# Performance work log

Hardware: AMD Instinct MI355X
Metric: run time of the kernel (lower is better)

Reference implementation:

```python
import jax, jax.numpy as jnp
import numpy as np


def conv3d(x, w, b, pad):
    # x: (B,C,D,H,W), w: (O,I,kd,kh,kw)
    y = jax.lax.conv_general_dilated(
        x, w, window_strides=(1, 1, 1), padding=[(pad, pad)] * 3,
        dimension_numbers=('NCDHW', 'OIDHW', 'NCDHW'))
    return y + b[None, :, None, None, None]


def setup_inputs() -> dict:
    key = jax.random.key(0)
    ks = jax.random.split(key, 8)
    B, C, D, H, W = 8, 128, 16, 32, 32
    C8 = C // 8
    return {
        'x': jax.random.normal(ks[0], (B, C, D, H, W), dtype=jnp.float32),
        'gamma': jax.random.normal(ks[1], (1,), dtype=jnp.float32),
        'w_k': jax.random.normal(ks[2], (C8, C, 1, 1, 1), dtype=jnp.float32) * 0.05,
        'b_k': jax.random.normal(ks[3], (C8,), dtype=jnp.float32) * 0.05,
        'w_q': jax.random.normal(ks[4], (C8, C, 1, 1, 1), dtype=jnp.float32) * 0.05,
        'b_q': jax.random.normal(ks[5], (C8,), dtype=jnp.float32) * 0.05,
        'w_v': jax.random.normal(ks[6], (C, C, 3, 3, 3), dtype=jnp.float32) * 0.02,
        'b_v': jax.random.normal(ks[7], (C,), dtype=jnp.float32) * 0.05,
    }


def reference(x, gamma, w_k, b_k, w_q, b_q, w_v, b_v):
    B, C, D, H, W = x.shape
    HW = H * W
    k = conv3d(x, w_k, b_k, 0)   # (B, C/8, D, H, W)
    q = conv3d(x, w_q, b_q, 0)   # (B, C/8, D, H, W)
    v = conv3d(x, w_v, b_v, 1)   # (B, C, D, H, W)

    # --- spatial (P) attention over HW positions, feature dim (C/8)*D ---
    kf = k.reshape(B, -1, HW)
    qf = q.reshape(B, -1, HW)
    # cor[b,s,t] = sum_f k[b,f,s] q[b,f,t]; softmax over t
    A_p = jax.nn.softmax(jnp.einsum('bfs,bft->bst', kf, qf), axis=-1)  # (B,HW,HW)
    vf = v.reshape(B, C * D, HW)
    # Patt[b,m,j] = sum_t v[b,m,t] A_p[b,j,t]  (v @ A_p^T)
    Patt = jnp.einsum('bmt,bjt->bmj', vf, A_p).reshape(B, C, D, H, W)

    # --- depth (D) attention over D slices, feature dim (C/8)*H*W ---
    kd = k.transpose(0, 2, 1, 3, 4).reshape(B, D, -1)
    qd = q.transpose(0, 2, 1, 3, 4).reshape(B, D, -1)
    A_d = jax.nn.softmax(jnp.einsum('bdf,bef->bde', kd, qd), axis=-1)  # (B,D,D)
    vd = v.transpose(0, 2, 1, 3, 4).reshape(B, D, -1)  # (B, D, C*H*W)
    # Datt[b,j,f] = sum_d A_d[b,j,d] vd[b,d,f]
    Datt = jnp.einsum('bjd,bdf->bjf', A_d, vd).reshape(B, D, C, H, W)
    Datt = Datt.transpose(0, 2, 1, 3, 4)  # (B,C,D,H,W)

    return gamma[0] * (Patt + Datt) + x
```

## Files before the change

### kernel.cpp

```cpp
#include <hip/hip_runtime.h>

#define HW   1024
#define DHW  16384

typedef __attribute__((ext_vector_type(8))) short short8;
typedef __attribute__((ext_vector_type(4))) float f32x4;

static __device__ __forceinline__ ushort f2bf(float f) {
  unsigned u = __float_as_uint(f);
  unsigned r = (u + 0x7fffu + ((u >> 16) & 1u)) >> 16;
  return (ushort)r;
}
static __device__ __forceinline__ float bf2f(ushort u) {
  return __uint_as_float(((unsigned)u) << 16);
}
static __device__ __forceinline__ void async_copy16(const ushort* g, ushort* l) {
  __builtin_amdgcn_global_load_lds(
      (const __attribute__((address_space(1))) unsigned int*)g,
      (__attribute__((address_space(3))) unsigned int*)l, 16, 0, 0);
}

__global__ __launch_bounds__(256) void kq_kernel(
    const float* __restrict__ x, const float* __restrict__ wk,
    const float* __restrict__ bk, const float* __restrict__ wq,
    const float* __restrict__ bq, float* __restrict__ k, float* __restrict__ q) {
  __shared__ float wks[16 * 128];
  __shared__ float wqs[16 * 128];
  int tid = threadIdx.x;
  for (int i = tid; i < 2048; i += 256) { wks[i] = wk[i]; wqs[i] = wq[i]; }
  __syncthreads();
  int b = blockIdx.y;
  int p = blockIdx.x * 256 + tid;
  float ak[16], aq[16];
#pragma unroll
  for (int o = 0; o < 16; ++o) { ak[o] = 0.f; aq[o] = 0.f; }
  const float* xb = x + (size_t)b * 128 * DHW + p;
  for (int c = 0; c < 128; ++c) {
    float xv = xb[(size_t)c * DHW];
#pragma unroll
    for (int o = 0; o < 16; ++o) {
      ak[o] += wks[o * 128 + c] * xv;
      aq[o] += wqs[o * 128 + c] * xv;
    }
  }
#pragma unroll
  for (int o = 0; o < 16; ++o) {
    k[((size_t)b * 16 + o) * DHW + p] = ak[o] + bk[o];
    q[((size_t)b * 16 + o) * DHW + p] = aq[o] + bq[o];
  }
}

__global__ __launch_bounds__(256) void wprep_kernel(
    const float* __restrict__ wv, ushort* __restrict__ wt,
    ushort* __restrict__ zbuf) {
  if (blockIdx.x == 0 && threadIdx.x < 512) zbuf[threadIdx.x] = 0;
  int i = blockIdx.x * 256 + threadIdx.x;
  if (i >= 27 * 128 * 128) return;
  int c8 = i & 7;
  int t = i >> 3;
  int o = t & 127; t >>= 7;
  int tap = t % 9; t /= 9;
  int chunk = t & 15;
  int kd = t >> 4;
  wt[i] = f2bf(wv[(size_t)(o * 128 + chunk * 8 + c8) * 27 + kd * 9 + tap]);
}

__global__ __launch_bounds__(256) void xprep_kernel(
    const float* __restrict__ x, ushort* __restrict__ xt) {
  __shared__ __align__(16) ushort tile[32 * 136];
  int tid = threadIdx.x;
  int bz = blockIdx.y;
  int b = bz >> 4, z = bz & 15;
  int p0 = blockIdx.x * 32;
  for (int i = tid; i < 4096; i += 256) {
    int c = i >> 5, p = i & 31;
    tile[p * 136 + c] = f2bf(x[((size_t)(b * 128 + c) * 16 + z) * 1024 + p0 + p]);
  }
  __syncthreads();
  for (int i = tid; i < 512; i += 256) {
    int chunk = i >> 5, p = i & 31;
    uint4 val = *(const uint4*)&tile[p * 136 + chunk * 8];
    *(uint4*)&xt[(((size_t)bz * 16 + chunk) * 1024 + p0 + p) * 8] = val;
  }
}

__global__ __launch_bounds__(256, 2) void vconv_mfma_kernel(
    const ushort* __restrict__ xt, const ushort* __restrict__ wt,
    const float* __restrict__ bv, const ushort* __restrict__ zbuf,
    ushort* __restrict__ v) {
  __shared__ __align__(16) ushort xs[1536 * 8];
  __shared__ __align__(16) ushort wsm[2304 * 8];
  int tid = threadIdx.x;
  int wave = tid >> 6;
  int ml = tid & 15;
  int quad = (tid >> 4) & 3;
  int bz = blockIdx.x;
  int b = bz & 7, z = bz >> 3;
  int h0 = blockIdx.y * 8;
  int o0 = blockIdx.z * 64;

  f32x4 acc[4][4];
#pragma unroll
  for (int s = 0; s < 4; ++s)
#pragma unroll
    for (int t = 0; t < 4; ++t) acc[s][t] = (f32x4){0.f, 0.f, 0.f, 0.f};

  int cb0[4];
#pragma unroll
  for (int t = 0; t < 4; ++t)
    cb0[t] = (wave * 2 + (t >> 1)) * 34 + (t & 1) * 16 + ml;

  int xoff[6]; bool okx[6];
#pragma unroll
  for (int it = 0; it < 6; ++it) {
    int i = it * 256 + tid;
    int cu = i / 340;
    int cell = i - cu * 340;
    int hr = cell / 34;
    int wc = cell - hr * 34;
    int h = h0 + hr - 1, ww = wc - 1;
    okx[it] = (i < 1360) && ((unsigned)h < 32u) && ((unsigned)ww < 32u);
    xoff[it] = cu * 1024 + h * 32 + ww;
  }
  int woff[9];
#pragma unroll
  for (int it = 0; it < 9; ++it) {
    int i = it * 256 + tid;
    int cu = i / 576;
    int r = i - cu * 576;
    int tap = r >> 6, ol = r & 63;
    woff[it] = (cu * 9 + tap) * 128 + o0 + ol;
  }

  const int KH[9] = {0, 0, 0, 1, 1, 1, 2, 2, 2};
  const int KW[9] = {0, 1, 2, 0, 1, 2, 0, 1, 2};

  for (int kd = 0; kd < 3; ++kd) {
    int zd = z + kd - 1;
    bool zok = (zd >= 0 && zd < 16);
    int zdc = zok ? zd : 0;
    const ushort* xbase = xt + (size_t)(b * 16 + zdc) * 16 * 1024 * 8;
    for (int cb = 0; cb < 4; ++cb) {
      const ushort* xsb = xbase + (size_t)cb * 4 * 1024 * 8;
      const ushort* wsb = wt + (size_t)(kd * 16 + cb * 4) * 9 * 128 * 8;
#pragma unroll
      for (int it = 0; it < 6; ++it) {
        const ushort* g = (zok && okx[it]) ? xsb + (size_t)xoff[it] * 8 : zbuf;
        async_copy16(g, &xs[(it * 256 + tid) * 8]);
      }
#pragma unroll
      for (int it = 0; it < 9; ++it)
        async_copy16(wsb + (size_t)woff[it] * 8, &wsm[(it * 256 + tid) * 8]);
      __syncthreads();
#pragma unroll
      for (int tap = 0; tap < 9; ++tap) {
        const int kh = KH[tap], kw = KW[tap];
        short8 af[4], bfr[4];
#pragma unroll
        for (int s = 0; s < 4; ++s)
          af[s] = *(const short8*)&wsm[(quad * 576 + tap * 64 + s * 16 + ml) * 8];
#pragma unroll
        for (int t = 0; t < 4; ++t) {
          int cell = cb0[t] + kh * 34 + kw;
          bfr[t] = *(const short8*)&xs[(quad * 340 + cell) * 8];
        }
#pragma unroll
        for (int s = 0; s < 4; ++s)
#pragma unroll
          for (int t = 0; t < 4; ++t)
            acc[s][t] = __builtin_amdgcn_mfma_f32_16x16x32_bf16(af[s], bfr[t], acc[s][t], 0, 0, 0);
      }
      __syncthreads();
    }
  }
#pragma unroll
  for (int s = 0; s < 4; ++s) {
    int o = o0 + s * 16 + quad * 4;
#pragma unroll
    for (int t = 0; t < 4; ++t) {
      int pl = wave * 64 + t * 16 + ml;
      ushort* dst = &v[((size_t)(b * 128 + o) * 16 + z) * 1024 + h0 * 32 + pl];
#pragma unroll
      for (int r = 0; r < 4; ++r)
        dst[(size_t)r * 16384] = f2bf(acc[s][t][r] + bv[o + r]);
    }
  }
}

__global__ __launch_bounds__(256) void kqt_kernel(
    const float* __restrict__ k, const float* __restrict__ q,
    ushort* __restrict__ kT, ushort* __restrict__ qT,
    float* __restrict__ rsum) {
  __shared__ __align__(16) ushort tile[32 * 264];
  int tid = threadIdx.x;
  int t0 = blockIdx.x;
  int b = blockIdx.y;
  if (t0 == 0)
    *(float4*)&rsum[b * 1024 + tid * 4] = (float4){0.f, 0.f, 0.f, 0.f};
  int h0 = t0 * 32;

  {
    const float* s = k + (size_t)b * 16 * DHW;
    for (int it = 0; it < 32; ++it) {
      int i = it * 256 + tid;
      int oo = i >> 9, zz = (i >> 5) & 15, hl = i & 31;
      tile[hl * 264 + oo * 16 + zz] =
          f2bf(s[(size_t)oo * DHW + zz * 1024 + h0 + hl]);
    }
    __syncthreads();
    ushort* d = kT + ((size_t)b * 1024 + h0) * 256;
    for (int jt = 0; jt < 4; ++jt) {
      int j = jt * 256 + tid;
      int hl = j >> 5, c8 = (j & 31) * 8;
      *(uint4*)&d[(size_t)hl * 256 + c8] = *(const uint4*)&tile[hl * 264 + c8];
    }
    __syncthreads();
  }
  {
    const float* s = q + (size_t)b * 16 * DHW;
    for (int it = 0; it < 32; ++it) {
      int i = it * 256 + tid;
      int oo = i >> 9, zz = (i >> 5) & 15, hl = i & 31;
      tile[hl * 264 + oo * 16 + zz] =
          f2bf(s[(size_t)oo * DHW + zz * 1024 + h0 + hl]);
    }
    __syncthreads();
    ushort* d = qT + ((size_t)b * 1024 + h0) * 256;
    for (int jt = 0; jt < 4; ++jt) {
      int j = jt * 256 + tid;
      int hl = j >> 5, c8 = (j & 31) * 8;
      *(uint4*)&d[(size_t)hl * 256 + c8] = *(const uint4*)&tile[hl * 264 + c8];
    }
  }
}

__global__ __launch_bounds__(256, 2) void apx_kernel(
    const ushort* __restrict__ kT, const ushort* __restrict__ qT,
    ushort* __restrict__ A_p, float* __restrict__ rsum) {
  __shared__ __align__(16) ushort smem[32768];
  int tid = threadIdx.x;
  int wave = tid >> 6, lane = tid & 63;
  int ml = lane & 15, quad = lane >> 4;
  int wm = wave >> 1, wj = wave & 1;
  int b = blockIdx.x;
  int tile = blockIdx.y;
  int m0 = (tile >> 3) * 128;
  int j0 = (tile & 7) * 128;

  f32x4 acc[4][4];
#pragma unroll
  for (int s = 0; s < 4; ++s)
#pragma unroll
    for (int t = 0; t < 4; ++t) acc[s][t] = (f32x4){0.f, 0.f, 0.f, 0.f};

  const ushort* va = kT + ((size_t)b * 1024 + m0) * 256;
  const ushort* pa = qT + ((size_t)b * 1024 + j0) * 256;

  int srow[4], skc[4];
#pragma unroll
  for (int n = 0; n < 4; ++n) {
    int slot = wave * 256 + n * 64 + lane;
    srow[n] = slot >> 3;
    skc[n] = (slot & 7) ^ (srow[n] & 7);
  }

#pragma unroll
  for (int n = 0; n < 4; ++n) {
    async_copy16(va + (size_t)srow[n] * 256 + skc[n] * 8,
                 &smem[(wave * 256 + n * 64) * 8]);
    async_copy16(pa + (size_t)srow[n] * 256 + skc[n] * 8,
                 &smem[8192 + (wave * 256 + n * 64) * 8]);
  }
  __syncthreads();

  for (int t = 0; t < 4; ++t) {
    int cur = (t & 1) * 16384;
    int nxt = 16384 - cur;
    if (t < 3) {
      int kk = (t + 1) * 64;
#pragma unroll
      for (int n = 0; n < 4; ++n) {
        async_copy16(va + (size_t)srow[n] * 256 + kk + skc[n] * 8,
                     &smem[nxt + (wave * 256 + n * 64) * 8]);
        async_copy16(pa + (size_t)srow[n] * 256 + kk + skc[n] * 8,
                     &smem[nxt + 8192 + (wave * 256 + n * 64) * 8]);
      }
    }
#pragma unroll
    for (int ks = 0; ks < 2; ++ks) {
      short8 af[4], bfr[4];
#pragma unroll
      for (int s = 0; s < 4; ++s) {
        int row = wm * 64 + s * 16 + ml;
        int c = ks * 4 + quad;
        af[s] = *(const short8*)&smem[cur + (row * 8 + (c ^ (row & 7))) * 8];
      }
#pragma unroll
      for (int t2 = 0; t2 < 4; ++t2) {
        int row = wj * 64 + t2 * 16 + ml;
        int c = ks * 4 + quad;
        bfr[t2] = *(const short8*)&smem[cur + 8192 + (row * 8 + (c ^ (row & 7))) * 8];
      }
#pragma unroll
      for (int s = 0; s < 4; ++s)
#pragma unroll
        for (int t2 = 0; t2 < 4; ++t2)
          acc[s][t2] = __builtin_amdgcn_mfma_f32_16x16x32_bf16(af[s], bfr[t2], acc[s][t2], 0, 0, 0);
    }
    __syncthreads();
  }

#pragma unroll
  for (int s = 0; s < 4; ++s)
#pragma unroll
    for (int r = 0; r < 4; ++r) {
      float sum = 0.f;
#pragma unroll
      for (int t2 = 0; t2 < 4; ++t2) {
        float p = __expf(acc[s][t2][r]);
        acc[s][t2][r] = p;
        sum += p;
      }
      sum += __shfl_xor(sum, 1);
      sum += __shfl_xor(sum, 2);
      sum += __shfl_xor(sum, 4);
      sum += __shfl_xor(sum, 8);
      if (ml == 0) {
        int m = m0 + wm * 64 + s * 16 + quad * 4 + r;
        atomicAdd(&rsum[b * 1024 + m], sum);
      }
    }
#pragma unroll
  for (int s = 0; s < 4; ++s)
#pragma unroll
    for (int t2 = 0; t2 < 4; ++t2) {
      int j = j0 + wj * 64 + t2 * 16 + ml;
#pragma unroll
      for (int r = 0; r < 4; ++r) {
        int m = m0 + wm * 64 + s * 16 + quad * 4 + r;
        A_p[((size_t)b * 1024 + m) * 1024 + j] = f2bf(acc[s][t2][r]);
      }
    }
}

__global__ __launch_bounds__(256) void ad_kernel(
    const float* __restrict__ k, const float* __restrict__ q,
    float* __restrict__ A_d) {
  int tid = threadIdx.x;
  int b = blockIdx.x >> 4;
  int dj = blockIdx.x & 15;
  float acc[16];
#pragma unroll
  for (int e = 0; e < 16; ++e) acc[e] = 0.f;
  const float* kb = k + (size_t)b * 256 * HW;
  const float* qb = q + (size_t)b * 256 * HW;
  for (int f = tid; f < 16384; f += 256) {
    int oc = f >> 10, hw = f & 1023;
    float kv = kb[(oc * 16 + dj) * HW + hw];
#pragma unroll
    for (int e = 0; e < 16; ++e)
      acc[e] += kv * qb[(oc * 16 + e) * HW + hw];
  }
  __shared__ float sred[16][4];
  __shared__ float arow[16];
  __shared__ float prow[16];
  int lane = tid & 63, wid = tid >> 6;
#pragma unroll
  for (int e = 0; e < 16; ++e) {
    float s = acc[e];
    for (int off = 32; off >= 1; off >>= 1) s += __shfl_xor(s, off);
    if (lane == 0) sred[e][wid] = s;
  }
  __syncthreads();
  if (tid < 16) arow[tid] = sred[tid][0] + sred[tid][1] + sred[tid][2] + sred[tid][3];
  __syncthreads();
  if (tid < 16) {
    float m = arow[0];
    for (int e = 1; e < 16; ++e) m = fmaxf(m, arow[e]);
    prow[tid] = __expf(arow[tid] - m);
  }
  __syncthreads();
  if (tid < 16) {
    float s = 0.f;
    for (int e = 0; e < 16; ++e) s += prow[e];
    A_d[(size_t)b * 256 + dj * 16 + tid] = prow[tid] / s;
  }
}

__global__ __launch_bounds__(256, 2) void combine_mfma_kernel(
    const ushort* __restrict__ vb, const ushort* __restrict__ apb,
    const float* __restrict__ A_d, const float* __restrict__ rsum,
    const float* __restrict__ x, const float* __restrict__ gamma,
    float* __restrict__ out) {
  __shared__ __align__(16) ushort smem[32768];
  __shared__ float Adt[272];
  int tid = threadIdx.x;
  int wave = tid >> 6, lane = tid & 63;
  int ml = lane & 15, quad = lane >> 4;
  int wm = wave >> 1, wj = wave & 1;
  int b = blockIdx.x;
  int tile = blockIdx.y;
  int m0 = (tile >> 3) * 128;
  int j0 = (tile & 7) * 128;
  Adt[(tid & 15) * 17 + (tid >> 4)] = A_d[b * 256 + tid];

  f32x4 acc[4][4];
#pragma unroll
  for (int s = 0; s < 4; ++s)
#pragma unroll
    for (int t = 0; t < 4; ++t) acc[s][t] = (f32x4){0.f, 0.f, 0.f, 0.f};

  const ushort* va = vb + ((size_t)b * 2048 + m0) * 1024;
  const ushort* pa = apb + ((size_t)b * 1024 + j0) * 1024;

  int srow[4], skc[4];
#pragma unroll
  for (int n = 0; n < 4; ++n) {
    int slot = wave * 256 + n * 64 + lane;
    srow[n] = slot >> 3;
    skc[n] = (slot & 7) ^ (srow[n] & 7);
  }

#pragma unroll
  for (int n = 0; n < 4; ++n) {
    async_copy16(va + (size_t)srow[n] * 1024 + skc[n] * 8,
                 &smem[(wave * 256 + n * 64) * 8]);
    async_copy16(pa + (size_t)srow[n] * 1024 + skc[n] * 8,
                 &smem[8192 + (wave * 256 + n * 64) * 8]);
  }
  __syncthreads();

  for (int t = 0; t < 16; ++t) {
    int cur = (t & 1) * 16384;
    int nxt = 16384 - cur;
    if (t < 15) {
      int kk = (t + 1) * 64;
#pragma unroll
      for (int n = 0; n < 4; ++n) {
        async_copy16(va + (size_t)srow[n] * 1024 + kk + skc[n] * 8,
                     &smem[nxt + (wave * 256 + n * 64) * 8]);
        async_copy16(pa + (size_t)srow[n] * 1024 + kk + skc[n] * 8,
                     &smem[nxt + 8192 + (wave * 256 + n * 64) * 8]);
      }
    }
#pragma unroll
    for (int ks = 0; ks < 2; ++ks) {
      short8 af[4], bfr[4];
#pragma unroll
      for (int s = 0; s < 4; ++s) {
        int row = wm * 64 + s * 16 + ml;
        int c = ks * 4 + quad;
        af[s] = *(const short8*)&smem[cur + (row * 8 + (c ^ (row & 7))) * 8];
      }
#pragma unroll
      for (int t2 = 0; t2 < 4; ++t2) {
        int row = wj * 64 + t2 * 16 + ml;
        int c = ks * 4 + quad;
        bfr[t2] = *(const short8*)&smem[cur + 8192 + (row * 8 + (c ^ (row & 7))) * 8];
      }
#pragma unroll
      for (int s = 0; s < 4; ++s)
#pragma unroll
        for (int t2 = 0; t2 < 4; ++t2)
          acc[s][t2] = __builtin_amdgcn_mfma_f32_16x16x32_bf16(af[s], bfr[t2], acc[s][t2], 0, 0, 0);
    }
    __syncthreads();
  }

  float invr[4];
#pragma unroll
  for (int t2 = 0; t2 < 4; ++t2)
    invr[t2] = 1.f / rsum[b * 1024 + j0 + wj * 64 + t2 * 16 + ml];
#pragma unroll
  for (int s = 0; s < 4; ++s)
#pragma unroll
    for (int t2 = 0; t2 < 4; ++t2)
#pragma unroll
      for (int r = 0; r < 4; ++r) acc[s][t2][r] *= invr[t2];

  for (int i = tid; i < 2048; i += 256) {
    int row = i >> 4, jc = i & 15;
    uint4 val = *(const uint4*)&vb[((size_t)b * 2048 + m0 + row) * 1024 + j0 + jc * 8];
    *(uint4*)&smem[row * 136 + jc * 8] = val;
  }
  __syncthreads();

#pragma unroll
  for (int d = 0; d < 16; ++d) {
    float ar[4];
#pragma unroll
    for (int r = 0; r < 4; ++r) ar[r] = Adt[d * 17 + quad * 4 + r];
#pragma unroll
    for (int s = 0; s < 4; ++s) {
      const ushort* vrow = &smem[(wm * 64 + s * 16 + d) * 136];
#pragma unroll
      for (int t2 = 0; t2 < 4; ++t2) {
        float vv = bf2f(vrow[wj * 64 + t2 * 16 + ml]);
#pragma unroll
        for (int r = 0; r < 4; ++r) acc[s][t2][r] += ar[r] * vv;
      }
    }
  }

  float g = gamma[0];
#pragma unroll
  for (int s = 0; s < 4; ++s) {
#pragma unroll
    for (int t2 = 0; t2 < 4; ++t2) {
      int jrel = wj * 64 + t2 * 16 + ml;
#pragma unroll
      for (int r = 0; r < 4; ++r) {
        int m = m0 + wm * 64 + s * 16 + quad * 4 + r;
        size_t idx = ((size_t)b * 2048 + m) * 1024 + j0 + jrel;
        out[idx] = g * acc[s][t2][r] + x[idx];
      }
    }
  }
}

extern "C" void kernel_launch(void* const* d_in, const int* in_sizes, int n_in,
                              void* d_out, int out_size, void* d_ws, size_t ws_size,
                              hipStream_t stream) {
  const float* x     = (const float*)d_in[0];
  const float* gamma = (const float*)d_in[1];
  const float* w_k   = (const float*)d_in[2];
  const float* b_k   = (const float*)d_in[3];
  const float* w_q   = (const float*)d_in[4];
  const float* b_q   = (const float*)d_in[5];
  const float* w_v   = (const float*)d_in[6];
  const float* b_v   = (const float*)d_in[7];
  float* out = (float*)d_out;

  float* k    = (float*)d_ws;
  float* q    = k + 2097152;
  float* A_d  = q + 2097152;
  ushort* vbf = (ushort*)(A_d + 2048);
  ushort* apb = vbf + 16777216;
  ushort* wt  = apb + 8388608;
  ushort* zbuf = wt + 442368;
  ushort* xt  = zbuf + 512;
  ushort* kT16 = xt;
  ushort* qT16 = xt + 2097152;
  float* rsum  = (float*)(xt + 4194304);

  wprep_kernel<<<dim3(1728), 256, 0, stream>>>(w_v, wt, zbuf);
  xprep_kernel<<<dim3(32, 128), 256, 0, stream>>>(x, xt);
  kq_kernel<<<dim3(64, 8), 256, 0, stream>>>(x, w_k, b_k, w_q, b_q, k, q);
  vconv_mfma_kernel<<<dim3(128, 4, 2), 256, 0, stream>>>(xt, wt, b_v, zbuf, vbf);
  kqt_kernel<<<dim3(32, 8), 256, 0, stream>>>(k, q, kT16, qT16, rsum);
  apx_kernel<<<dim3(8, 64), 256, 0, stream>>>(kT16, qT16, apb, rsum);
  ad_kernel<<<dim3(128), 256, 0, stream>>>(k, q, A_d);
  combine_mfma_kernel<<<dim3(8, 128), 256, 0, stream>>>(vbf, apb, A_d, rsum, x, gamma, out);
}
```

Measured before the change: 397.8 us.

## Fuse bf16 x-transpose into kq kernel and enlarge conv tile height

```diff
diff --git a/kernel.cpp b/kernel.cpp
--- a/kernel.cpp
+++ b/kernel.cpp
@@ -23,7 +23,8 @@
 __global__ __launch_bounds__(256) void kq_kernel(
     const float* __restrict__ x, const float* __restrict__ wk,
     const float* __restrict__ bk, const float* __restrict__ wq,
-    const float* __restrict__ bq, float* __restrict__ k, float* __restrict__ q) {
+    const float* __restrict__ bq, float* __restrict__ k, float* __restrict__ q,
+    ushort* __restrict__ xt) {
   __shared__ float wks[16 * 128];
   __shared__ float wqs[16 * 128];
   int tid = threadIdx.x;
@@ -31,17 +32,26 @@
   __syncthreads();
   int b = blockIdx.y;
   int p = blockIdx.x * 256 + tid;
+  int z = p >> 10, hw = p & 1023;
   float ak[16], aq[16];
 #pragma unroll
   for (int o = 0; o < 16; ++o) { ak[o] = 0.f; aq[o] = 0.f; }
   const float* xb = x + (size_t)b * 128 * DHW + p;
-  for (int c = 0; c < 128; ++c) {
-    float xv = xb[(size_t)c * DHW];
-#pragma unroll
-    for (int o = 0; o < 16; ++o) {
-      ak[o] += wks[o * 128 + c] * xv;
-      aq[o] += wqs[o * 128 + c] * xv;
-    }
+  ushort* xtp = xt + (((size_t)(b * 16 + z) * 16) * 1024 + hw) * 8;
+  for (int chunk = 0; chunk < 16; ++chunk) {
+    ushort pack[8];
+#pragma unroll
+    for (int c8 = 0; c8 < 8; ++c8) {
+      int c = chunk * 8 + c8;
+      float xv = xb[(size_t)c * DHW];
+      pack[c8] = f2bf(xv);
+#pragma unroll
+      for (int o = 0; o < 16; ++o) {
+        ak[o] += wks[o * 128 + c] * xv;
+        aq[o] += wqs[o * 128 + c] * xv;
+      }
+    }
+    *(uint4*)&xtp[(size_t)chunk * 1024 * 8] = *(const uint4*)pack;
   }
 #pragma unroll
   for (int o = 0; o < 16; ++o) {
@@ -65,30 +75,11 @@
   wt[i] = f2bf(wv[(size_t)(o * 128 + chunk * 8 + c8) * 27 + kd * 9 + tap]);
 }
 
-__global__ __launch_bounds__(256) void xprep_kernel(
-    const float* __restrict__ x, ushort* __restrict__ xt) {
-  __shared__ __align__(16) ushort tile[32 * 136];
-  int tid = threadIdx.x;
-  int bz = blockIdx.y;
-  int b = bz >> 4, z = bz & 15;
-  int p0 = blockIdx.x * 32;
-  for (int i = tid; i < 4096; i += 256) {
-    int c = i >> 5, p = i & 31;
-    tile[p * 136 + c] = f2bf(x[((size_t)(b * 128 + c) * 16 + z) * 1024 + p0 + p]);
-  }
-  __syncthreads();
-  for (int i = tid; i < 512; i += 256) {
-    int chunk = i >> 5, p = i & 31;
-    uint4 val = *(const uint4*)&tile[p * 136 + chunk * 8];
-    *(uint4*)&xt[(((size_t)bz * 16 + chunk) * 1024 + p0 + p) * 8] = val;
-  }
-}
-
 __global__ __launch_bounds__(256, 2) void vconv_mfma_kernel(
     const ushort* __restrict__ xt, const ushort* __restrict__ wt,
     const float* __restrict__ bv, const ushort* __restrict__ zbuf,
     ushort* __restrict__ v) {
-  __shared__ __align__(16) ushort xs[1536 * 8];
+  __shared__ __align__(16) ushort xs[2560 * 8];
   __shared__ __align__(16) ushort wsm[2304 * 8];
   int tid = threadIdx.x;
   int wave = tid >> 6;
@@ -96,30 +87,30 @@
   int quad = (tid >> 4) & 3;
   int bz = blockIdx.x;
   int b = bz & 7, z = bz >> 3;
-  int h0 = blockIdx.y * 8;
+  int h0 = blockIdx.y * 16;
   int o0 = blockIdx.z * 64;
 
-  f32x4 acc[4][4];
+  f32x4 acc[4][8];
 #pragma unroll
   for (int s = 0; s < 4; ++s)
 #pragma unroll
-    for (int t = 0; t < 4; ++t) acc[s][t] = (f32x4){0.f, 0.f, 0.f, 0.f};
-
-  int cb0[4];
-#pragma unroll
-  for (int t = 0; t < 4; ++t)
-    cb0[t] = (wave * 2 + (t >> 1)) * 34 + (t & 1) * 16 + ml;
-
-  int xoff[6]; bool okx[6];
-#pragma unroll
-  for (int it = 0; it < 6; ++it) {
+    for (int t = 0; t < 8; ++t) acc[s][t] = (f32x4){0.f, 0.f, 0.f, 0.f};
+
+  int cb0[8];
+#pragma unroll
+  for (int t = 0; t < 8; ++t)
+    cb0[t] = (wave * 4 + (t >> 1)) * 34 + (t & 1) * 16 + ml;
+
+  int xoff[10]; bool okx[10];
+#pragma unroll
+  for (int it = 0; it < 10; ++it) {
     int i = it * 256 + tid;
-    int cu = i / 340;
-    int cell = i - cu * 340;
+    int cu = i / 612;
+    int cell = i - cu * 612;
     int hr = cell / 34;
     int wc = cell - hr * 34;
     int h = h0 + hr - 1, ww = wc - 1;
-    okx[it] = (i < 1360) && ((unsigned)h < 32u) && ((unsigned)ww < 32u);
+    okx[it] = (i < 2448) && ((unsigned)h < 32u) && ((unsigned)ww < 32u);
     xoff[it] = cu * 1024 + h * 32 + ww;
   }
   int woff[9];
@@ -144,7 +135,7 @@
       const ushort* xsb = xbase + (size_t)cb * 4 * 1024 * 8;
       const ushort* wsb = wt + (size_t)(kd * 16 + cb * 4) * 9 * 128 * 8;
 #pragma unroll
-      for (int it = 0; it < 6; ++it) {
+      for (int it = 0; it < 10; ++it) {
         const ushort* g = (zok && okx[it]) ? xsb + (size_t)xoff[it] * 8 : zbuf;
         async_copy16(g, &xs[(it * 256 + tid) * 8]);
       }
@@ -155,19 +146,19 @@
 #pragma unroll
       for (int tap = 0; tap < 9; ++tap) {
         const int kh = KH[tap], kw = KW[tap];
-        short8 af[4], bfr[4];
+        short8 af[4], bfr[8];
 #pragma unroll
         for (int s = 0; s < 4; ++s)
           af[s] = *(const short8*)&wsm[(quad * 576 + tap * 64 + s * 16 + ml) * 8];
 #pragma unroll
-        for (int t = 0; t < 4; ++t) {
+        for (int t = 0; t < 8; ++t) {
           int cell = cb0[t] + kh * 34 + kw;
-          bfr[t] = *(const short8*)&xs[(quad * 340 + cell) * 8];
+          bfr[t] = *(const short8*)&xs[(quad * 612 + cell) * 8];
         }
 #pragma unroll
         for (int s = 0; s < 4; ++s)
 #pragma unroll
-          for (int t = 0; t < 4; ++t)
+          for (int t = 0; t < 8; ++t)
             acc[s][t] = __builtin_amdgcn_mfma_f32_16x16x32_bf16(af[s], bfr[t], acc[s][t], 0, 0, 0);
       }
       __syncthreads();
@@ -177,8 +168,8 @@
   for (int s = 0; s < 4; ++s) {
     int o = o0 + s * 16 + quad * 4;
 #pragma unroll
-    for (int t = 0; t < 4; ++t) {
-      int pl = wave * 64 + t * 16 + ml;
+    for (int t = 0; t < 8; ++t) {
+      int pl = wave * 128 + t * 16 + ml;
       ushort* dst = &v[((size_t)(b * 128 + o) * 16 + z) * 1024 + h0 * 32 + pl];
 #pragma unroll
       for (int r = 0; r < 4; ++r)
@@ -544,9 +535,8 @@
   float* rsum  = (float*)(xt + 4194304);
 
   wprep_kernel<<<dim3(1728), 256, 0, stream>>>(w_v, wt, zbuf);
-  xprep_kernel<<<dim3(32, 128), 256, 0, stream>>>(x, xt);
-  kq_kernel<<<dim3(64, 8), 256, 0, stream>>>(x, w_k, b_k, w_q, b_q, k, q);
-  vconv_mfma_kernel<<<dim3(128, 4, 2), 256, 0, stream>>>(xt, wt, b_v, zbuf, vbf);
+  kq_kernel<<<dim3(64, 8), 256, 0, stream>>>(x, w_k, b_k, w_q, b_q, k, q, xt);
+  vconv_mfma_kernel<<<dim3(128, 2, 2), 256, 0, stream>>>(xt, wt, b_v, zbuf, vbf);
   kqt_kernel<<<dim3(32, 8), 256, 0, stream>>>(k, q, kT16, qT16, rsum);
   apx_kernel<<<dim3(8, 64), 256, 0, stream>>>(kT16, qT16, apb, rsum);
   ad_kernel<<<dim3(128), 256, 0, stream>>>(k, q, A_d);
```

New measurement: 423.3 us. 1.06x slower.

## Fuse bf16 transpose of x into kq kernel and split depth-attention reduction

Applied to the files above, without the earlier changes.

```diff
diff --git a/kernel.cpp b/kernel.cpp
--- a/kernel.cpp
+++ b/kernel.cpp
@@ -23,7 +23,8 @@
 __global__ __launch_bounds__(256) void kq_kernel(
     const float* __restrict__ x, const float* __restrict__ wk,
     const float* __restrict__ bk, const float* __restrict__ wq,
-    const float* __restrict__ bq, float* __restrict__ k, float* __restrict__ q) {
+    const float* __restrict__ bq, float* __restrict__ k, float* __restrict__ q,
+    ushort* __restrict__ xt) {
   __shared__ float wks[16 * 128];
   __shared__ float wqs[16 * 128];
   int tid = threadIdx.x;
@@ -31,17 +32,26 @@
   __syncthreads();
   int b = blockIdx.y;
   int p = blockIdx.x * 256 + tid;
+  int z = p >> 10, hw = p & 1023;
   float ak[16], aq[16];
 #pragma unroll
   for (int o = 0; o < 16; ++o) { ak[o] = 0.f; aq[o] = 0.f; }
   const float* xb = x + (size_t)b * 128 * DHW + p;
-  for (int c = 0; c < 128; ++c) {
-    float xv = xb[(size_t)c * DHW];
-#pragma unroll
-    for (int o = 0; o < 16; ++o) {
-      ak[o] += wks[o * 128 + c] * xv;
-      aq[o] += wqs[o * 128 + c] * xv;
-    }
+  ushort* xtp = xt + (((size_t)(b * 16 + z) * 16) * 1024 + hw) * 8;
+  for (int chunk = 0; chunk < 16; ++chunk) {
+    ushort pack[8];
+#pragma unroll
+    for (int c8 = 0; c8 < 8; ++c8) {
+      int c = chunk * 8 + c8;
+      float xv = xb[(size_t)c * DHW];
+      pack[c8] = f2bf(xv);
+#pragma unroll
+      for (int o = 0; o < 16; ++o) {
+        ak[o] += wks[o * 128 + c] * xv;
+        aq[o] += wqs[o * 128 + c] * xv;
+      }
+    }
+    *(uint4*)&xtp[(size_t)chunk * 1024 * 8] = *(const uint4*)pack;
   }
 #pragma unroll
   for (int o = 0; o < 16; ++o) {
@@ -63,25 +73,6 @@
   int chunk = t & 15;
   int kd = t >> 4;
   wt[i] = f2bf(wv[(size_t)(o * 128 + chunk * 8 + c8) * 27 + kd * 9 + tap]);
-}
-
-__global__ __launch_bounds__(256) void xprep_kernel(
-    const float* __restrict__ x, ushort* __restrict__ xt) {
-  __shared__ __align__(16) ushort tile[32 * 136];
-  int tid = threadIdx.x;
-  int bz = blockIdx.y;
-  int b = bz >> 4, z = bz & 15;
-  int p0 = blockIdx.x * 32;
-  for (int i = tid; i < 4096; i += 256) {
-    int c = i >> 5, p = i & 31;
-    tile[p * 136 + c] = f2bf(x[((size_t)(b * 128 + c) * 16 + z) * 1024 + p0 + p]);
-  }
-  __syncthreads();
-  for (int i = tid; i < 512; i += 256) {
-    int chunk = i >> 5, p = i & 31;
-    uint4 val = *(const uint4*)&tile[p * 136 + chunk * 8];
-    *(uint4*)&xt[(((size_t)bz * 16 + chunk) * 1024 + p0 + p) * 8] = val;
-  }
 }
 
 __global__ __launch_bounds__(256, 2) void vconv_mfma_kernel(
@@ -190,13 +181,15 @@
 __global__ __launch_bounds__(256) void kqt_kernel(
     const float* __restrict__ k, const float* __restrict__ q,
     ushort* __restrict__ kT, ushort* __restrict__ qT,
-    float* __restrict__ rsum) {
+    float* __restrict__ rsum, float* __restrict__ Sd) {
   __shared__ __align__(16) ushort tile[32 * 264];
   int tid = threadIdx.x;
   int t0 = blockIdx.x;
   int b = blockIdx.y;
-  if (t0 == 0)
+  if (t0 == 0) {
     *(float4*)&rsum[b * 1024 + tid * 4] = (float4){0.f, 0.f, 0.f, 0.f};
+    Sd[b * 256 + tid] = 0.f;
+  }
   int h0 = t0 * 32;
 
   {
@@ -343,48 +336,48 @@
     }
 }
 
-__global__ __launch_bounds__(256) void ad_kernel(
+__global__ __launch_bounds__(256) void ad_part_kernel(
     const float* __restrict__ k, const float* __restrict__ q,
-    float* __restrict__ A_d) {
+    float* __restrict__ Sd) {
   int tid = threadIdx.x;
-  int b = blockIdx.x >> 4;
-  int dj = blockIdx.x & 15;
+  int b = blockIdx.x;
+  int dj = blockIdx.y;
+  int split = blockIdx.z;
   float acc[16];
 #pragma unroll
   for (int e = 0; e < 16; ++e) acc[e] = 0.f;
   const float* kb = k + (size_t)b * 256 * HW;
   const float* qb = q + (size_t)b * 256 * HW;
-  for (int f = tid; f < 16384; f += 256) {
+  int fend = (split + 1) * 4096;
+  for (int f = split * 4096 + tid; f < fend; f += 256) {
     int oc = f >> 10, hw = f & 1023;
     float kv = kb[(oc * 16 + dj) * HW + hw];
 #pragma unroll
     for (int e = 0; e < 16; ++e)
       acc[e] += kv * qb[(oc * 16 + e) * HW + hw];
   }
-  __shared__ float sred[16][4];
-  __shared__ float arow[16];
-  __shared__ float prow[16];
-  int lane = tid & 63, wid = tid >> 6;
+  int lane = tid & 63;
 #pragma unroll
   for (int e = 0; e < 16; ++e) {
     float s = acc[e];
     for (int off = 32; off >= 1; off >>= 1) s += __shfl_xor(s, off);
-    if (lane == 0) sred[e][wid] = s;
-  }
-  __syncthreads();
-  if (tid < 16) arow[tid] = sred[tid][0] + sred[tid][1] + sred[tid][2] + sred[tid][3];
-  __syncthreads();
-  if (tid < 16) {
-    float m = arow[0];
-    for (int e = 1; e < 16; ++e) m = fmaxf(m, arow[e]);
-    prow[tid] = __expf(arow[tid] - m);
-  }
-  __syncthreads();
-  if (tid < 16) {
-    float s = 0.f;
-    for (int e = 0; e < 16; ++e) s += prow[e];
-    A_d[(size_t)b * 256 + dj * 16 + tid] = prow[tid] / s;
-  }
+    if (lane == 0) atomicAdd(&Sd[b * 256 + dj * 16 + e], s);
+  }
+}
+
+__global__ __launch_bounds__(128) void ad_fin_kernel(
+    const float* __restrict__ Sd, float* __restrict__ A_d) {
+  int t = threadIdx.x;
+  const float* row = Sd + (size_t)t * 16;
+  float m = row[0];
+#pragma unroll
+  for (int e = 1; e < 16; ++e) m = fmaxf(m, row[e]);
+  float p[16], s = 0.f;
+#pragma unroll
+  for (int e = 0; e < 16; ++e) { p[e] = __expf(row[e] - m); s += p[e]; }
+  float inv = 1.f / s;
+#pragma unroll
+  for (int e = 0; e < 16; ++e) A_d[(size_t)t * 16 + e] = p[e] * inv;
 }
 
 __global__ __launch_bounds__(256, 2) void combine_mfma_kernel(
@@ -542,13 +535,14 @@
   ushort* kT16 = xt;
   ushort* qT16 = xt + 2097152;
   float* rsum  = (float*)(xt + 4194304);
+  float* Sd    = rsum + 8192;
 
   wprep_kernel<<<dim3(1728), 256, 0, stream>>>(w_v, wt, zbuf);
-  xprep_kernel<<<dim3(32, 128), 256, 0, stream>>>(x, xt);
-  kq_kernel<<<dim3(64, 8), 256, 0, stream>>>(x, w_k, b_k, w_q, b_q, k, q);
+  kq_kernel<<<dim3(64, 8), 256, 0, stream>>>(x, w_k, b_k, w_q, b_q, k, q, xt);
   vconv_mfma_kernel<<<dim3(128, 4, 2), 256, 0, stream>>>(xt, wt, b_v, zbuf, vbf);
-  kqt_kernel<<<dim3(32, 8), 256, 0, stream>>>(k, q, kT16, qT16, rsum);
+  kqt_kernel<<<dim3(32, 8), 256, 0, stream>>>(k, q, kT16, qT16, rsum, Sd);
   apx_kernel<<<dim3(8, 64), 256, 0, stream>>>(kT16, qT16, apb, rsum);
-  ad_kernel<<<dim3(128), 256, 0, stream>>>(k, q, A_d);
+  ad_part_kernel<<<dim3(8, 16, 4), 256, 0, stream>>>(k, q, Sd);
+  ad_fin_kernel<<<dim3(1), 128, 0, stream>>>(Sd, A_d);
   combine_mfma_kernel<<<dim3(8, 128), 256, 0, stream>>>(vbf, apb, A_d, rsum, x, gamma, out);
 }
```

After: 374.0 us. 6.0% less time.
